# Optimization experiments

Measured on AMD Instinct MI355X. Metric: run time of the kernel, lower is better.

The kernel has to match this reference:

```python
import jax, jax.numpy as jnp
import numpy as np

INPUT_DIM = 512
LATENT_DIM = 64
H1, H2 = 128, 64  # hardcoded hidden widths in Encoder/Decoder
BATCH = 4096


def _xavier(key, shape):
    fan_out, fan_in = shape
    std = jnp.sqrt(2.0 / (fan_in + fan_out))
    return std * jax.random.normal(key, shape, dtype=jnp.float32)


def setup_inputs() -> dict:
    key = jax.random.key(0)
    ks = jax.random.split(key, 10)
    d = LATENT_DIM
    n_pairs = d * (d - 1) // 2
    n_funcs = 1 + d + n_pairs  # bias + states + pairwise products
    inp = {
        "x": jax.random.normal(ks[0], (BATCH, INPUT_DIM), dtype=jnp.float32),
        "xdot": jax.random.normal(ks[1], (BATCH, INPUT_DIM), dtype=jnp.float32),
        # encoder weights (torch Linear layout: [out, in])
        "We1": _xavier(ks[2], (H1, INPUT_DIM)), "be1": jnp.zeros((H1,), jnp.float32),
        "We2": _xavier(ks[3], (H2, H1)),        "be2": jnp.zeros((H2,), jnp.float32),
        "We3": _xavier(ks[4], (d, H2)),         "be3": jnp.zeros((d,), jnp.float32),
        # decoder weights
        "Wd1": _xavier(ks[5], (H2, d)),         "bd1": jnp.zeros((H2,), jnp.float32),
        "Wd2": _xavier(ks[6], (H1, H2)),        "bd2": jnp.zeros((H1,), jnp.float32),
        "Wd3": _xavier(ks[7], (INPUT_DIM, H1)), "bd3": jnp.zeros((INPUT_DIM,), jnp.float32),
        "XI": jnp.ones((n_funcs, d), jnp.float32),
        "XI_mask": jnp.ones((n_funcs, d), jnp.float32),
    }
    return inp


def _mlp_with_jacobian(x, Ws, bs):
    """3-layer relu MLP; returns output and per-sample analytic Jacobian [B,out,in].
    Jacobian = diag(m3) W3 diag(m2) W2 diag(m1) W1 with relu masks m_l."""
    h = x
    J = None
    for W, b in zip(Ws, bs):
        h = h @ W.T + b                      # [B, out_l]
        m = (h > 0).astype(h.dtype)          # relu mask (grad 0 at 0, matching torch)
        h = jnp.maximum(h, 0)
        Wm = m[:, :, None] * W[None]         # [B, out_l, in_l]
        J = Wm if J is None else jnp.einsum('boh,bhi->boi', Wm, J)
    return h, J


def _sindy_library(z):
    B, d = z.shape
    iu, ju = np.triu_indices(d, k=1)
    ones = jnp.ones((B, 1), z.dtype)
    pairs = z[:, iu] * z[:, ju]              # [B, d(d-1)/2]
    return jnp.concatenate([ones, z, pairs], axis=1)


def reference(x, xdot, We1, be1, We2, be2, We3, be3,
              Wd1, bd1, Wd2, bd2, Wd3, bd3, XI, XI_mask):
    z, Jenc = _mlp_with_jacobian(x, (We1, We2, We3), (be1, be2, be3))
    dz_dt = jnp.einsum('bli,bi->bl', Jenc, xdot)
    xh, Jdec = _mlp_with_jacobian(z, (Wd1, Wd2, Wd3), (bd1, bd2, bd3))
    theta = _sindy_library(z)
    dz_dt_sindy = theta @ (XI_mask * XI)
    dxh_dt = jnp.einsum('bol,bl->bo', Jdec, dz_dt_sindy)
    return (xh, dxh_dt, z, dz_dt, dz_dt_sindy)
```

## Files before the change

kernel.cpp:

```cpp
#include <hip/hip_runtime.h>

#define BATCH 4096
#define IN_DIM 512
#define H1DIM 128
#define H2DIM 64
#define DDIM 64
#define NFUNC 2081
#define NFPAD 2112
#define CHUNK 704
#define KS_PER_CHUNK 22

typedef short bf16x8 __attribute__((ext_vector_type(8)));
typedef float f32x4 __attribute__((ext_vector_type(4)));
#define MFMA(a,b,c) __builtin_amdgcn_mfma_f32_16x16x32_bf16(a,b,c,0,0,0)

#define WSZ1 (H1DIM*IN_DIM)
#define WSZ2 (H2DIM*H1DIM)
#define WSZ3 (DDIM*H2DIM)
#define WSZ4 (H2DIM*DDIM)
#define WSZ5 (H1DIM*H2DIM)
#define WSZ6 (IN_DIM*H1DIM)

__device__ __forceinline__ short f2b(float f) {
    union { float f; unsigned u; } x; x.f = f;
    unsigned r = x.u + 0x7fffu + ((x.u >> 16) & 1u);
    return (short)(r >> 16);
}
__device__ __forceinline__ float b2f(short s) {
    union { unsigned u; float f; } x; x.u = ((unsigned)(unsigned short)s) << 16;
    return x.f;
}
__device__ __forceinline__ void split3f(float v, short& s0, short& s1, short& s2) {
    s0 = f2b(v); float r = v - b2f(s0);
    s1 = f2b(r); float r2 = r - b2f(s1);
    s2 = f2b(r2);
}

__device__ __forceinline__ void st_b16(short* t, int RS, int r, int c, short v) {
    int b = (c * 2) ^ ((r & 7) << 4);
    *(short*)((char*)(t + r * RS) + b) = v;
}
__device__ __forceinline__ void st_b32s(short* t, int RS, int r, int c, unsigned v) {
    int b = (c * 2) ^ ((r & 7) << 4);
    *(unsigned*)((char*)(t + r * RS) + b) = v;
}
__device__ __forceinline__ void st_b128(short* t, int RS, int r, int c0, bf16x8 v) {
    int b = (c0 * 2) ^ ((r & 7) << 4);
    *(bf16x8*)((char*)(t + r * RS) + b) = v;
}
__device__ __forceinline__ bf16x8 ld_af(const short* t, int RS, int lane, int kbase) {
    int r = lane & 15;
    int b = ((kbase + (lane >> 4) * 8) * 2) ^ ((r & 7) << 4);
    return *(const bf16x8*)((const char*)(t + r * RS) + b);
}
__device__ __forceinline__ bf16x8 ld_bp(const short* P, int blk, int lane) {
    return *(const bf16x8*)(P + ((size_t)blk * 64 + lane) * 8);
}

__device__ __forceinline__ void mf9(bf16x8 f0, bf16x8 f1, bf16x8 f2, bf16x8 fv,
                                    bf16x8 b0, bf16x8 b1, bf16x8 b2,
                                    f32x4& P, f32x4& Q, f32x4& V) {
    P = MFMA(f0, b0, P); Q = MFMA(f1, b1, Q);
    P = MFMA(f1, b0, P); Q = MFMA(f0, b1, Q);
    P = MFMA(f2, b0, P); Q = MFMA(f2, b1, Q);
    P = MFMA(f0, b2, P); Q = MFMA(f1, b2, Q);
    V = MFMA(fv, b0, V);
}

__device__ __forceinline__ void epi_store(short* t0, short* t1, short* t2, short* tv, int RS,
                                          int lane, int col, const f32x4& P, const f32x4& Q,
                                          const f32x4& V, float bb)
{
    #pragma unroll
    for (int q = 0; q < 4; ++q) {
        int row = (lane >> 4) * 4 + q;
        float pre = P[q] + Q[q] + bb;
        float h = fmaxf(pre, 0.f);
        short s0, s1, s2;
        split3f(h, s0, s1, s2);
        st_b16(t0, RS, row, col, s0);
        st_b16(t1, RS, row, col, s1);
        st_b16(t2, RS, row, col, s2);
        st_b16(tv, RS, row, col, pre > 0.f ? f2b(V[q]) : (short)0);
    }
}

template<int K>
__device__ void pack_w(const float* __restrict__ W, short* __restrict__ dst, int NK,
                       int gid, int nthr)
{
    for (int o = gid; o < NK / 8; o += nthr) {
        int c = o / (K / 8), k0 = (o - c * (K / 8)) * 8;
        int cb = c >> 4, ks = k0 >> 5;
        int L = (((k0 >> 3) & 3) << 4) | (c & 15);
        int idx = ((cb * (K / 32) + ks) * 64 + L) * 8;
        union { short s[8]; bf16x8 v; } p0, p1, p2;
        #pragma unroll
        for (int j = 0; j < 8; ++j)
            split3f(W[(size_t)c * K + k0 + j], p0.s[j], p1.s[j], p2.s[j]);
        *(bf16x8*)(dst + idx) = p0.v;
        *(bf16x8*)(dst + NK + idx) = p1.v;
        *(bf16x8*)(dst + 2 * NK + idx) = p2.v;
    }
}

__global__ void initk(const float* __restrict__ We1, const float* __restrict__ We2,
                      const float* __restrict__ We3, const float* __restrict__ Wd1,
                      const float* __restrict__ Wd2, const float* __restrict__ Wd3,
                      const float* __restrict__ XI, const float* __restrict__ XIm,
                      short* Wp1, short* Wp2, short* Wp3, short* Wp4, short* Wp5, short* Wp6,
                      short* xiP, int2* pk)
{
    int gid = blockIdx.x * blockDim.x + threadIdx.x;
    int nthr = gridDim.x * blockDim.x;

    pack_w<512>(We1, Wp1, WSZ1, gid, nthr);
    pack_w<128>(We2, Wp2, WSZ2, gid, nthr);
    pack_w<64>(We3, Wp3, WSZ3, gid, nthr);
    pack_w<64>(Wd1, Wp4, WSZ4, gid, nthr);
    pack_w<64>(Wd2, Wp5, WSZ5, gid, nthr);
    pack_w<128>(Wd3, Wp6, WSZ6, gid, nthr);

    for (int i = gid; i < 4 * 66 * 64; i += nthr) {
        int cb = i / (66 * 64);
        int r = i - cb * (66 * 64);
        int ks = r >> 6, L = r & 63;
        int col = cb * 16 + (L & 15);
        union { short s[8]; bf16x8 v; } w;
        #pragma unroll
        for (int j = 0; j < 8; ++j) {
            int f = ks * 32 + ((L >> 4) << 3) + j;
            float v = (f < NFUNC) ? XI[(size_t)f * DDIM + col] * XIm[(size_t)f * DDIM + col] : 0.f;
            w.s[j] = f2b(v);
        }
        *(bf16x8*)(xiP + (size_t)i * 8) = w.v;
    }

    for (int f = gid; f < NFPAD; f += nthr) {
        int a, b;
        if (f == 0) { a = 64; b = 64; }
        else if (f <= DDIM) { a = f - 1; b = 64; }
        else if (f < NFUNC) {
            int p = f - 1 - DDIM; int i2 = 0, cum = 0;
            while (cum + (63 - i2) <= p) { cum += 63 - i2; ++i2; }
            a = i2; b = i2 + 1 + (p - cum);
        } else { a = 65; b = 65; }
        pk[f] = make_int2(a, b);
    }
}

__global__ __launch_bounds__(512, 2)
void fused(const float* __restrict__ x, const float* __restrict__ xdot,
           const float* __restrict__ be1, const float* __restrict__ be2,
           const float* __restrict__ be3, const float* __restrict__ bd1,
           const float* __restrict__ bd2, const float* __restrict__ bd3,
           const short* __restrict__ Wp1, const short* __restrict__ Wp2,
           const short* __restrict__ Wp3, const short* __restrict__ Wp4,
           const short* __restrict__ Wp5, const short* __restrict__ Wp6,
           const short* __restrict__ xiP, const int2* __restrict__ pk,
           float* __restrict__ xh, float* __restrict__ dxh, float* __restrict__ zo,
           float* __restrict__ dz, float* __restrict__ dzs)
{
    __shared__ __align__(16) char ldsbuf[57600];
    short* h1s0 = (short*)(ldsbuf + 0);
    short* h1s1 = (short*)(ldsbuf + 4096);
    short* h1s2 = (short*)(ldsbuf + 8192);
    short* v1   = (short*)(ldsbuf + 12288);
    short* xs0  = (short*)(ldsbuf + 16384);
    short* xs1  = (short*)(ldsbuf + 24576);
    short* xs2  = (short*)(ldsbuf + 32768);
    short* xsv  = (short*)(ldsbuf + 40960);
    short* h2s0 = (short*)(ldsbuf + 16384);
    short* h2s1 = (short*)(ldsbuf + 18432);
    short* h2s2 = (short*)(ldsbuf + 20480);
    short* v2   = (short*)(ldsbuf + 22528);
    short* th0  = (short*)(ldsbuf + 0);
    short* th1  = (short*)(ldsbuf + 22528);
    float* rbuf = (float*)(ldsbuf + 16384);
    short* g1s0 = (short*)(ldsbuf + 0);
    short* g1s1 = (short*)(ldsbuf + 2048);
    short* g1s2 = (short*)(ldsbuf + 4096);
    short* u1   = (short*)(ldsbuf + 6144);
    short* g2s0 = (short*)(ldsbuf + 8192);
    short* g2s1 = (short*)(ldsbuf + 12288);
    short* g2s2 = (short*)(ldsbuf + 16384);
    short* u2   = (short*)(ldsbuf + 20480);
    short* zb0  = (short*)(ldsbuf + 45056);
    short* zb1  = (short*)(ldsbuf + 47104);
    short* zb2  = (short*)(ldsbuf + 49152);
    short* dzsb = (short*)(ldsbuf + 51200);
    float* zf   = (float*)(ldsbuf + 53248);

    const int tid = threadIdx.x, lane = tid & 63, wave = tid >> 6;
    const int wq = wave & 3;
    const int row0 = blockIdx.x * 16;
    const int c16 = lane & 15;
    const int tr = tid & 15, bg = tid >> 4;
    const int tf = bg * 22;
    const int scb = wave & 3, skh = wave >> 2;

    float bb1 = be1[wave * 16 + c16];
    float bb2 = be2[wq * 16 + c16];
    float bb3 = be3[wq * 16 + c16];
    float bD1 = bd1[wq * 16 + c16];
    float bD2 = bd2[wave * 16 + c16];
    float bD3[4];
    #pragma unroll
    for (int i = 0; i < 4; ++i) bD3[i] = bd3[wave * 64 + i * 16 + c16];

    f32x4 P1 = {}, Q1 = {}, V1 = {};
    {
        const int srow = tid >> 5, sc0 = (tid & 31) * 8;
        const float* xr  = x    + (size_t)(row0 + srow) * IN_DIM + sc0;
        const float* xdr = xdot + (size_t)(row0 + srow) * IN_DIM + sc0;
        #pragma clang loop unroll(disable)
        for (int h = 0; h < 2; ++h) {
            {
                f32x4 va = *(const f32x4*)(xr + h * 256);
                f32x4 vb = *(const f32x4*)(xr + h * 256 + 4);
                f32x4 da = *(const f32x4*)(xdr + h * 256);
                f32x4 db = *(const f32x4*)(xdr + h * 256 + 4);
                union { short s[8]; bf16x8 v; } a0, a1, a2, dv;
                #pragma unroll
                for (int j = 0; j < 4; ++j) {
                    split3f(va[j], a0.s[j], a1.s[j], a2.s[j]);
                    split3f(vb[j], a0.s[j + 4], a1.s[j + 4], a2.s[j + 4]);
                    dv.s[j] = f2b(da[j]); dv.s[j + 4] = f2b(db[j]);
                }
                st_b128(xs0, 256, srow, sc0, a0.v);
                st_b128(xs1, 256, srow, sc0, a1.v);
                st_b128(xs2, 256, srow, sc0, a2.v);
                st_b128(xsv, 256, srow, sc0, dv.v);
            }
            __syncthreads();
            bf16x8 B0[2], B1[2], B2[2];
#define LB(ks, sl) { int blk = wave * 16 + h * 8 + (ks); \
            B0[sl] = ld_bp(Wp1, blk, lane); B1[sl] = ld_bp(Wp1 + WSZ1, blk, lane); \
            B2[sl] = ld_bp(Wp1 + 2 * WSZ1, blk, lane); }
            LB(0, 0)
            #pragma unroll
            for (int ks = 0; ks < 8; ++ks) {
                if (ks < 7) LB(ks + 1, (ks + 1) & 1)
                bf16x8 f0 = ld_af(xs0, 256, lane, ks * 32);
                bf16x8 f1 = ld_af(xs1, 256, lane, ks * 32);
                bf16x8 f2 = ld_af(xs2, 256, lane, ks * 32);
                bf16x8 fv = ld_af(xsv, 256, lane, ks * 32);
                mf9(f0, f1, f2, fv, B0[ks & 1], B1[ks & 1], B2[ks & 1], P1, Q1, V1);
            }
#undef LB
            __syncthreads();
        }
        epi_store(h1s0, h1s1, h1s2, v1, 128, lane, wave * 16 + c16, P1, Q1, V1, bb1);
    }
    bf16x8 L2B[4][3];
    if (wave < 4) {
        #pragma unroll
        for (int ks = 0; ks < 4; ++ks) {
            int blk = wq * 4 + ks;
            L2B[ks][0] = ld_bp(Wp2, blk, lane);
            L2B[ks][1] = ld_bp(Wp2 + WSZ2, blk, lane);
            L2B[ks][2] = ld_bp(Wp2 + 2 * WSZ2, blk, lane);
        }
    }
    __syncthreads();

    bf16x8 L3B[2][3];
    if (wave < 4) {
        bf16x8 Aa[4][4];
        #pragma unroll
        for (int ks = 0; ks < 4; ++ks) {
            Aa[ks][0] = ld_af(h1s0, 128, lane, ks * 32);
            Aa[ks][1] = ld_af(h1s1, 128, lane, ks * 32);
            Aa[ks][2] = ld_af(h1s2, 128, lane, ks * 32);
            Aa[ks][3] = ld_af(v1, 128, lane, ks * 32);
        }
        #pragma unroll
        for (int ks = 0; ks < 2; ++ks) {
            int blk = wq * 2 + ks;
            L3B[ks][0] = ld_bp(Wp3, blk, lane);
            L3B[ks][1] = ld_bp(Wp3 + WSZ3, blk, lane);
            L3B[ks][2] = ld_bp(Wp3 + 2 * WSZ3, blk, lane);
        }
        f32x4 P = {}, Q = {}, V = {};
        #pragma unroll
        for (int ks = 0; ks < 4; ++ks)
            mf9(Aa[ks][0], Aa[ks][1], Aa[ks][2], Aa[ks][3], L2B[ks][0], L2B[ks][1], L2B[ks][2], P, Q, V);
        epi_store(h2s0, h2s1, h2s2, v2, 64, lane, wq * 16 + c16, P, Q, V, bb2);
    }
    __syncthreads();

    bf16x8 X[11];
    if (wave < 4) {
        bf16x8 Aa[2][4];
        #pragma unroll
        for (int ks = 0; ks < 2; ++ks) {
            Aa[ks][0] = ld_af(h2s0, 64, lane, ks * 32);
            Aa[ks][1] = ld_af(h2s1, 64, lane, ks * 32);
            Aa[ks][2] = ld_af(h2s2, 64, lane, ks * 32);
            Aa[ks][3] = ld_af(v2, 64, lane, ks * 32);
        }
        f32x4 P = {}, Q = {}, V = {};
        #pragma unroll
        for (int ks = 0; ks < 2; ++ks)
            mf9(Aa[ks][0], Aa[ks][1], Aa[ks][2], Aa[ks][3], L3B[ks][0], L3B[ks][1], L3B[ks][2], P, Q, V);
        int col = wq * 16 + c16;
        #pragma unroll
        for (int q = 0; q < 4; ++q) {
            int row = (lane >> 4) * 4 + q;
            float pre = P[q] + Q[q] + bb3;
            float hz = fmaxf(pre, 0.f);
            float vz = pre > 0.f ? V[q] : 0.f;
            zf[row * 68 + col] = hz;
            short s0, s1, s2;
            split3f(hz, s0, s1, s2);
            st_b16(zb0, 64, row, col, s0);
            st_b16(zb1, 64, row, col, s1);
            st_b16(zb2, 64, row, col, s2);
            zo[(size_t)(row0 + row) * DDIM + col] = hz;
            dz[(size_t)(row0 + row) * DDIM + col] = vz;
        }
        if (tid < 32) { int r = tid & 15; zf[r * 68 + 64 + (tid >> 4)] = (tid >> 4) ? 0.f : 1.f; }
    }
    #pragma unroll
    for (int kk = 0; kk < 11; ++kk)
        X[kk] = ld_bp(xiP, scb * 66 + skh * 11 + kk, lane);
    __syncthreads();

    f32x4 sa = {};
    auto build = [&](int ch, short* t) {
        #pragma clang loop unroll(disable)
        for (int j = 0; j < 11; ++j) {
            int f0 = ch * CHUNK + tf + 2 * j;
            int2 p0 = pk[f0], p1 = pk[f0 + 1];
            float t0 = zf[tr * 68 + p0.x] * zf[tr * 68 + p0.y];
            float t1 = zf[tr * 68 + p1.x] * zf[tr * 68 + p1.y];
            unsigned u = (unsigned)(unsigned short)f2b(t0)
                       | ((unsigned)(unsigned short)f2b(t1) << 16);
            st_b32s(t, 704, tr, tf + 2 * j, u);
        }
    };
#define SMF(t) { _Pragma("unroll") for (int kk = 0; kk < 11; ++kk) { \
        bf16x8 a = ld_af(t, 704, lane, (skh * 11 + kk) * 32); \
        sa = MFMA(a, X[kk], sa); } }
#define ISX(ch) { _Pragma("unroll") for (int kk = 0; kk < 11; ++kk) \
        X[kk] = ld_bp(xiP, scb * 66 + (ch) * KS_PER_CHUNK + skh * 11 + kk, lane); }

    build(0, th0);
    __syncthreads();
    SMF(th0) ISX(1) build(1, th1);
    __syncthreads();
    SMF(th1) ISX(2) build(2, th0);
    __syncthreads();
    SMF(th0)
    if (wave >= 4) *(f32x4*)&rbuf[(scb * 64 + lane) * 4] = sa;
    __syncthreads();
    bf16x8 D1B[2][3];
    if (wave < 4) {
        f32x4 sacc = sa + *(const f32x4*)&rbuf[(scb * 64 + lane) * 4];
        #pragma unroll
        for (int ks = 0; ks < 2; ++ks) {
            int blk = wq * 2 + ks;
            D1B[ks][0] = ld_bp(Wp4, blk, lane);
            D1B[ks][1] = ld_bp(Wp4 + WSZ4, blk, lane);
            D1B[ks][2] = ld_bp(Wp4 + 2 * WSZ4, blk, lane);
        }
        int col = wq * 16 + c16;
        #pragma unroll
        for (int q = 0; q < 4; ++q) {
            int row = (lane >> 4) * 4 + q;
            float v = sacc[q];
            dzs[(size_t)(row0 + row) * DDIM + col] = v;
            st_b16(dzsb, 64, row, col, f2b(v));
        }
    }
#undef SMF
#undef ISX
    __syncthreads();

    bf16x8 D2B[2][3];
    if (wave < 4) {
        bf16x8 Aa[2][4];
        #pragma unroll
        for (int ks = 0; ks < 2; ++ks) {
            Aa[ks][0] = ld_af(zb0, 64, lane, ks * 32);
            Aa[ks][1] = ld_af(zb1, 64, lane, ks * 32);
            Aa[ks][2] = ld_af(zb2, 64, lane, ks * 32);
            Aa[ks][3] = ld_af(dzsb, 64, lane, ks * 32);
        }
        f32x4 P = {}, Q = {}, V = {};
        #pragma unroll
        for (int ks = 0; ks < 2; ++ks)
            mf9(Aa[ks][0], Aa[ks][1], Aa[ks][2], Aa[ks][3], D1B[ks][0], D1B[ks][1], D1B[ks][2], P, Q, V);
        epi_store(g1s0, g1s1, g1s2, u1, 64, lane, wq * 16 + c16, P, Q, V, bD1);
    }
    #pragma unroll
    for (int ks = 0; ks < 2; ++ks) {
        int blk = wave * 2 + ks;
        D2B[ks][0] = ld_bp(Wp5, blk, lane);
        D2B[ks][1] = ld_bp(Wp5 + WSZ5, blk, lane);
        D2B[ks][2] = ld_bp(Wp5 + 2 * WSZ5, blk, lane);
    }
    __syncthreads();

    {
        bf16x8 Aa[2][4];
        #pragma unroll
        for (int ks = 0; ks < 2; ++ks) {
            Aa[ks][0] = ld_af(g1s0, 64, lane, ks * 32);
            Aa[ks][1] = ld_af(g1s1, 64, lane, ks * 32);
            Aa[ks][2] = ld_af(g1s2, 64, lane, ks * 32);
            Aa[ks][3] = ld_af(u1, 64, lane, ks * 32);
        }
        f32x4 P = {}, Q = {}, V = {};
        #pragma unroll
        for (int ks = 0; ks < 2; ++ks)
            mf9(Aa[ks][0], Aa[ks][1], Aa[ks][2], Aa[ks][3], D2B[ks][0], D2B[ks][1], D2B[ks][2], P, Q, V);
        epi_store(g2s0, g2s1, g2s2, u2, 128, lane, wave * 16 + c16, P, Q, V, bD2);
    }
    __syncthreads();

    {
        f32x4 P[4] = {}, Q[4] = {}, V[4] = {};
        bf16x8 Bp[4][3];
        bf16x8 Ax0[2], Ax1[2], Ax2[2], Axv[2];
#define D3_LA(ks, b) { Ax0[b] = ld_af(g2s0, 128, lane, (ks) * 32); Ax1[b] = ld_af(g2s1, 128, lane, (ks) * 32); \
                       Ax2[b] = ld_af(g2s2, 128, lane, (ks) * 32); Axv[b] = ld_af(u2, 128, lane, (ks) * 32); }
#define D3_LB(s, sl) { int blk = (wave * 4 + ((s) & 3)) * 4 + ((s) >> 2); \
        Bp[sl][0] = ld_bp(Wp6, blk, lane); Bp[sl][1] = ld_bp(Wp6 + WSZ6, blk, lane); \
        Bp[sl][2] = ld_bp(Wp6 + 2 * WSZ6, blk, lane); }
        D3_LA(0, 0)
        D3_LB(0, 0) D3_LB(1, 1) D3_LB(2, 2) D3_LB(3, 3)
        #pragma unroll
        for (int ks = 0; ks < 4; ++ks) {
            if (ks < 3) D3_LA(ks + 1, (ks + 1) & 1)
            #pragma unroll
            for (int cf = 0; cf < 4; ++cf) {
                const int s = ks * 4 + cf, sl = s & 3;
                mf9(Ax0[ks & 1], Ax1[ks & 1], Ax2[ks & 1], Axv[ks & 1],
                    Bp[sl][0], Bp[sl][1], Bp[sl][2], P[cf], Q[cf], V[cf]);
                if (s + 4 < 16) D3_LB(s + 4, sl)
            }
        }
#undef D3_LA
#undef D3_LB
        #pragma unroll
        for (int cf = 0; cf < 4; ++cf) {
            int col = wave * 64 + cf * 16 + c16;
            float bb = bD3[cf];
            #pragma unroll
            for (int q = 0; q < 4; ++q) {
                int row = (lane >> 4) * 4 + q;
                float pre = P[cf][q] + Q[cf][q] + bb;
                xh[(size_t)(row0 + row) * IN_DIM + col] = fmaxf(pre, 0.f);
                dxh[(size_t)(row0 + row) * IN_DIM + col] = pre > 0.f ? V[cf][q] : 0.f;
            }
        }
    }
}

extern "C" void kernel_launch(void* const* d_in, const int* in_sizes, int n_in,
                              void* d_out, int out_size, void* d_ws, size_t ws_size,
                              hipStream_t stream)
{
    const float* x    = (const float*)d_in[0];
    const float* xdot = (const float*)d_in[1];
    const float* We1  = (const float*)d_in[2];
    const float* be1  = (const float*)d_in[3];
    const float* We2  = (const float*)d_in[4];
    const float* be2  = (const float*)d_in[5];
    const float* We3  = (const float*)d_in[6];
    const float* be3  = (const float*)d_in[7];
    const float* Wd1  = (const float*)d_in[8];
    const float* bd1  = (const float*)d_in[9];
    const float* Wd2  = (const float*)d_in[10];
    const float* bd2  = (const float*)d_in[11];
    const float* Wd3  = (const float*)d_in[12];
    const float* bd3  = (const float*)d_in[13];
    const float* XI   = (const float*)d_in[14];
    const float* XIm  = (const float*)d_in[15];

    float* out = (float*)d_out;
    float* xh  = out;
    float* dxh = out + (size_t)BATCH * IN_DIM;
    float* zo  = dxh + (size_t)BATCH * IN_DIM;
    float* dz  = zo + (size_t)BATCH * DDIM;
    float* dzs = dz + (size_t)BATCH * DDIM;

    int2*  pk  = (int2*)d_ws;
    short* Wp1 = (short*)(pk + NFPAD);
    short* Wp2 = Wp1 + 3 * WSZ1;
    short* Wp3 = Wp2 + 3 * WSZ2;
    short* Wp4 = Wp3 + 3 * WSZ3;
    short* Wp5 = Wp4 + 3 * WSZ4;
    short* Wp6 = Wp5 + 3 * WSZ5;
    short* xiP = Wp6 + 3 * WSZ6;

    initk<<<256, 256, 0, stream>>>(We1, We2, We3, Wd1, Wd2, Wd3, XI, XIm,
                                   Wp1, Wp2, Wp3, Wp4, Wp5, Wp6, xiP, pk);
    fused<<<BATCH / 16, 512, 0, stream>>>(x, xdot, be1, be2, be3, bd1, bd2, bd3,
                                          Wp1, Wp2, Wp3, Wp4, Wp5, Wp6, xiP, pk,
                                          xh, dxh, zo, dz, dzs);
}
```

Measured before the change: 42.90 us.

## Prefetch both input halves upfront and split layer-2 K across all eight waves

All global loads of x and xdot for both K-halves of layer 1 are now issued at the start instead of inside the loop, so the second half's memory latency overlaps with the first half's MFMA work. Layer 2 previously ran on only four waves. It now splits the K dimension across all eight waves, and partial accumulators from the upper waves are reduced through an LDS scratch buffer. This costs more live registers, an extra LDS round-trip and an extra barrier.

Result: no change. 42.66 us (-0.6%).

```diff
diff --git a/kernel.cpp b/kernel.cpp
--- a/kernel.cpp
+++ b/kernel.cpp
@@ -177,6 +177,7 @@
     short* th0  = (short*)(ldsbuf + 0);
     short* th1  = (short*)(ldsbuf + 22528);
     float* rbuf = (float*)(ldsbuf + 16384);
+    float* l2rb = (float*)(ldsbuf + 32768);
     short* g1s0 = (short*)(ldsbuf + 0);
     short* g1s1 = (short*)(ldsbuf + 2048);
     short* g1s2 = (short*)(ldsbuf + 4096);
@@ -213,79 +214,98 @@
         const int srow = tid >> 5, sc0 = (tid & 31) * 8;
         const float* xr  = x    + (size_t)(row0 + srow) * IN_DIM + sc0;
         const float* xdr = xdot + (size_t)(row0 + srow) * IN_DIM + sc0;
-        #pragma clang loop unroll(disable)
-        for (int h = 0; h < 2; ++h) {
-            {
-                f32x4 va = *(const f32x4*)(xr + h * 256);
-                f32x4 vb = *(const f32x4*)(xr + h * 256 + 4);
-                f32x4 da = *(const f32x4*)(xdr + h * 256);
-                f32x4 db = *(const f32x4*)(xdr + h * 256 + 4);
-                union { short s[8]; bf16x8 v; } a0, a1, a2, dv;
-                #pragma unroll
-                for (int j = 0; j < 4; ++j) {
-                    split3f(va[j], a0.s[j], a1.s[j], a2.s[j]);
-                    split3f(vb[j], a0.s[j + 4], a1.s[j + 4], a2.s[j + 4]);
-                    dv.s[j] = f2b(da[j]); dv.s[j + 4] = f2b(db[j]);
-                }
-                st_b128(xs0, 256, srow, sc0, a0.v);
-                st_b128(xs1, 256, srow, sc0, a1.v);
-                st_b128(xs2, 256, srow, sc0, a2.v);
-                st_b128(xsv, 256, srow, sc0, dv.v);
+        f32x4 va0 = *(const f32x4*)(xr);        f32x4 vb0 = *(const f32x4*)(xr + 4);
+        f32x4 da0 = *(const f32x4*)(xdr);       f32x4 db0 = *(const f32x4*)(xdr + 4);
+        f32x4 va1 = *(const f32x4*)(xr + 256);  f32x4 vb1 = *(const f32x4*)(xr + 260);
+        f32x4 da1 = *(const f32x4*)(xdr + 256); f32x4 db1 = *(const f32x4*)(xdr + 260);
+
+#define L1_STAGE(va, vb, da, db) { \
+        union { short s[8]; bf16x8 v; } a0, a1, a2, dv; \
+        _Pragma("unroll") \
+        for (int j = 0; j < 4; ++j) { \
+            split3f((va)[j], a0.s[j], a1.s[j], a2.s[j]); \
+            split3f((vb)[j], a0.s[j + 4], a1.s[j + 4], a2.s[j + 4]); \
+            dv.s[j] = f2b((da)[j]); dv.s[j + 4] = f2b((db)[j]); \
+        } \
+        st_b128(xs0, 256, srow, sc0, a0.v); \
+        st_b128(xs1, 256, srow, sc0, a1.v); \
+        st_b128(xs2, 256, srow, sc0, a2.v); \
+        st_b128(xsv, 256, srow, sc0, dv.v); }
+
+#define L1_COMP(h) { \
+        bf16x8 B0[2], B1[2], B2[2]; \
+        { int blk = wave * 16 + (h) * 8; \
+          B0[0] = ld_bp(Wp1, blk, lane); B1[0] = ld_bp(Wp1 + WSZ1, blk, lane); \
+          B2[0] = ld_bp(Wp1 + 2 * WSZ1, blk, lane); } \
+        _Pragma("unroll") \
+        for (int ks = 0; ks < 8; ++ks) { \
+            if (ks < 7) { int blk = wave * 16 + (h) * 8 + ks + 1; \
+                B0[(ks + 1) & 1] = ld_bp(Wp1, blk, lane); \
+                B1[(ks + 1) & 1] = ld_bp(Wp1 + WSZ1, blk, lane); \
+                B2[(ks + 1) & 1] = ld_bp(Wp1 + 2 * WSZ1, blk, lane); } \
+            bf16x8 f0 = ld_af(xs0, 256, lane, ks * 32); \
+            bf16x8 f1 = ld_af(xs1, 256, lane, ks * 32); \
+            bf16x8 f2 = ld_af(xs2, 256, lane, ks * 32); \
+            bf16x8 fv = ld_af(xsv, 256, lane, ks * 32); \
+            mf9(f0, f1, f2, fv, B0[ks & 1], B1[ks & 1], B2[ks & 1], P1, Q1, V1); \
+        } }
+
+        L1_STAGE(va0, vb0, da0, db0)
+        __syncthreads();
+        L1_COMP(0)
+        __syncthreads();
+        L1_STAGE(va1, vb1, da1, db1)
+        __syncthreads();
+        L1_COMP(1)
+        __syncthreads();
+#undef L1_STAGE
+#undef L1_COMP
+        epi_store(h1s0, h1s1, h1s2, v1, 128, lane, wave * 16 + c16, P1, Q1, V1, bb1);
+    }
+    bf16x8 L2B[2][3];
+    #pragma unroll
+    for (int ks = 0; ks < 2; ++ks) {
+        int blk = wq * 4 + (wave >> 2) * 2 + ks;
+        L2B[ks][0] = ld_bp(Wp2, blk, lane);
+        L2B[ks][1] = ld_bp(Wp2 + WSZ2, blk, lane);
+        L2B[ks][2] = ld_bp(Wp2 + 2 * WSZ2, blk, lane);
+    }
+    __syncthreads();
+
+    bf16x8 L3B[2][3];
+    {
+        const int kh = wave >> 2;
+        f32x4 P = {}, Q = {}, V = {};
+        #pragma unroll
+        for (int ks = 0; ks < 2; ++ks) {
+            int kg = kh * 2 + ks;
+            bf16x8 a0 = ld_af(h1s0, 128, lane, kg * 32);
+            bf16x8 a1 = ld_af(h1s1, 128, lane, kg * 32);
+            bf16x8 a2 = ld_af(h1s2, 128, lane, kg * 32);
+            bf16x8 av = ld_af(v1, 128, lane, kg * 32);
+            mf9(a0, a1, a2, av, L2B[ks][0], L2B[ks][1], L2B[ks][2], P, Q, V);
+        }
+        if (kh == 1) {
+            float* rb = l2rb + (wq * 64 + lane) * 12;
+            *(f32x4*)(rb) = P; *(f32x4*)(rb + 4) = Q; *(f32x4*)(rb + 8) = V;
+        }
+        if (wave < 4) {
+            #pragma unroll
+            for (int ks = 0; ks < 2; ++ks) {
+                int blk = wq * 2 + ks;
+                L3B[ks][0] = ld_bp(Wp3, blk, lane);
+                L3B[ks][1] = ld_bp(Wp3 + WSZ3, blk, lane);
+                L3B[ks][2] = ld_bp(Wp3 + 2 * WSZ3, blk, lane);
             }
-            __syncthreads();
-            bf16x8 B0[2], B1[2], B2[2];
-#define LB(ks, sl) { int blk = wave * 16 + h * 8 + (ks); \
-            B0[sl] = ld_bp(Wp1, blk, lane); B1[sl] = ld_bp(Wp1 + WSZ1, blk, lane); \
-            B2[sl] = ld_bp(Wp1 + 2 * WSZ1, blk, lane); }
-            LB(0, 0)
-            #pragma unroll
-            for (int ks = 0; ks < 8; ++ks) {
-                if (ks < 7) LB(ks + 1, (ks + 1) & 1)
-                bf16x8 f0 = ld_af(xs0, 256, lane, ks * 32);
-                bf16x8 f1 = ld_af(xs1, 256, lane, ks * 32);
-                bf16x8 f2 = ld_af(xs2, 256, lane, ks * 32);
-                bf16x8 fv = ld_af(xsv, 256, lane, ks * 32);
-                mf9(f0, f1, f2, fv, B0[ks & 1], B1[ks & 1], B2[ks & 1], P1, Q1, V1);
-            }
-#undef LB
-            __syncthreads();
-        }
-        epi_store(h1s0, h1s1, h1s2, v1, 128, lane, wave * 16 + c16, P1, Q1, V1, bb1);
-    }
-    bf16x8 L2B[4][3];
-    if (wave < 4) {
-        #pragma unroll
-        for (int ks = 0; ks < 4; ++ks) {
-            int blk = wq * 4 + ks;
-            L2B[ks][0] = ld_bp(Wp2, blk, lane);
-            L2B[ks][1] = ld_bp(Wp2 + WSZ2, blk, lane);
-            L2B[ks][2] = ld_bp(Wp2 + 2 * WSZ2, blk, lane);
-        }
-    }
-    __syncthreads();
-
-    bf16x8 L3B[2][3];
-    if (wave < 4) {
-        bf16x8 Aa[4][4];
-        #pragma unroll
-        for (int ks = 0; ks < 4; ++ks) {
-            Aa[ks][0] = ld_af(h1s0, 128, lane, ks * 32);
-            Aa[ks][1] = ld_af(h1s1, 128, lane, ks * 32);
-            Aa[ks][2] = ld_af(h1s2, 128, lane, ks * 32);
-            Aa[ks][3] = ld_af(v1, 128, lane, ks * 32);
-        }
-        #pragma unroll
-        for (int ks = 0; ks < 2; ++ks) {
-            int blk = wq * 2 + ks;
-            L3B[ks][0] = ld_bp(Wp3, blk, lane);
-            L3B[ks][1] = ld_bp(Wp3 + WSZ3, blk, lane);
-            L3B[ks][2] = ld_bp(Wp3 + 2 * WSZ3, blk, lane);
-        }
-        f32x4 P = {}, Q = {}, V = {};
-        #pragma unroll
-        for (int ks = 0; ks < 4; ++ks)
-            mf9(Aa[ks][0], Aa[ks][1], Aa[ks][2], Aa[ks][3], L2B[ks][0], L2B[ks][1], L2B[ks][2], P, Q, V);
-        epi_store(h2s0, h2s1, h2s2, v2, 64, lane, wq * 16 + c16, P, Q, V, bb2);
+        }
+        __syncthreads();
+        if (wave < 4) {
+            const float* rb = l2rb + (wq * 64 + lane) * 12;
+            f32x4 P2 = P + *(const f32x4*)(rb);
+            f32x4 Q2 = Q + *(const f32x4*)(rb + 4);
+            f32x4 V2 = V + *(const f32x4*)(rb + 8);
+            epi_store(h2s0, h2s1, h2s2, v2, 64, lane, wq * 16 + c16, P2, Q2, V2, bb2);
+        }
     }
     __syncthreads();
 
```

## Stage full 512-wide input tile in LDS at once, removing K-half loop

Applied to the files above, without the earlier changes.

The first layer used to stage x/xdot in two 256-column halves, with a barrier pair per half. It now issues all global loads for both halves up front and converts them to bf16 splits into a full 512-wide LDS tile. It then runs a single 16-step MFMA loop. LDS is enlarged to 64 KB and all buffers are remapped to fit, removing one round of barriers and exposing more memory-level parallelism at the cost of more registers and LDS, which may reduce occupancy below two blocks per CU.

After: 42.46 us (median of 2 runs). Within noise of the previous version (-1.0%).

```diff
diff --git a/kernel.cpp b/kernel.cpp
--- a/kernel.cpp
+++ b/kernel.cpp
@@ -161,22 +161,27 @@
            float* __restrict__ xh, float* __restrict__ dxh, float* __restrict__ zo,
            float* __restrict__ dz, float* __restrict__ dzs)
 {
-    __shared__ __align__(16) char ldsbuf[57600];
+    __shared__ __align__(16) char ldsbuf[65536];
+    short* xs0  = (short*)(ldsbuf + 0);
+    short* xs1  = (short*)(ldsbuf + 16384);
+    short* xs2  = (short*)(ldsbuf + 32768);
+    short* xsv  = (short*)(ldsbuf + 49152);
     short* h1s0 = (short*)(ldsbuf + 0);
     short* h1s1 = (short*)(ldsbuf + 4096);
     short* h1s2 = (short*)(ldsbuf + 8192);
     short* v1   = (short*)(ldsbuf + 12288);
-    short* xs0  = (short*)(ldsbuf + 16384);
-    short* xs1  = (short*)(ldsbuf + 24576);
-    short* xs2  = (short*)(ldsbuf + 32768);
-    short* xsv  = (short*)(ldsbuf + 40960);
     short* h2s0 = (short*)(ldsbuf + 16384);
     short* h2s1 = (short*)(ldsbuf + 18432);
     short* h2s2 = (short*)(ldsbuf + 20480);
     short* v2   = (short*)(ldsbuf + 22528);
-    short* th0  = (short*)(ldsbuf + 0);
-    short* th1  = (short*)(ldsbuf + 22528);
-    float* rbuf = (float*)(ldsbuf + 16384);
+    short* zb0  = (short*)(ldsbuf + 24576);
+    short* zb1  = (short*)(ldsbuf + 26624);
+    short* zb2  = (short*)(ldsbuf + 28672);
+    short* dzsb = (short*)(ldsbuf + 30720);
+    float* zf   = (float*)(ldsbuf + 32768);
+    short* th0  = (short*)(ldsbuf + 37888);
+    short* th1  = (short*)(ldsbuf + 0);
+    float* rbuf = (float*)(ldsbuf + 60416);
     short* g1s0 = (short*)(ldsbuf + 0);
     short* g1s1 = (short*)(ldsbuf + 2048);
     short* g1s2 = (short*)(ldsbuf + 4096);
@@ -185,11 +190,6 @@
     short* g2s1 = (short*)(ldsbuf + 12288);
     short* g2s2 = (short*)(ldsbuf + 16384);
     short* u2   = (short*)(ldsbuf + 20480);
-    short* zb0  = (short*)(ldsbuf + 45056);
-    short* zb1  = (short*)(ldsbuf + 47104);
-    short* zb2  = (short*)(ldsbuf + 49152);
-    short* dzsb = (short*)(ldsbuf + 51200);
-    float* zf   = (float*)(ldsbuf + 53248);
 
     const int tid = threadIdx.x, lane = tid & 63, wave = tid >> 6;
     const int wq = wave & 3;
@@ -213,43 +213,58 @@
         const int srow = tid >> 5, sc0 = (tid & 31) * 8;
         const float* xr  = x    + (size_t)(row0 + srow) * IN_DIM + sc0;
         const float* xdr = xdot + (size_t)(row0 + srow) * IN_DIM + sc0;
-        #pragma clang loop unroll(disable)
-        for (int h = 0; h < 2; ++h) {
-            {
-                f32x4 va = *(const f32x4*)(xr + h * 256);
-                f32x4 vb = *(const f32x4*)(xr + h * 256 + 4);
-                f32x4 da = *(const f32x4*)(xdr + h * 256);
-                f32x4 db = *(const f32x4*)(xdr + h * 256 + 4);
-                union { short s[8]; bf16x8 v; } a0, a1, a2, dv;
-                #pragma unroll
-                for (int j = 0; j < 4; ++j) {
-                    split3f(va[j], a0.s[j], a1.s[j], a2.s[j]);
-                    split3f(vb[j], a0.s[j + 4], a1.s[j + 4], a2.s[j + 4]);
-                    dv.s[j] = f2b(da[j]); dv.s[j + 4] = f2b(db[j]);
-                }
-                st_b128(xs0, 256, srow, sc0, a0.v);
-                st_b128(xs1, 256, srow, sc0, a1.v);
-                st_b128(xs2, 256, srow, sc0, a2.v);
-                st_b128(xsv, 256, srow, sc0, dv.v);
+        f32x4 va0 = *(const f32x4*)(xr);        f32x4 vb0 = *(const f32x4*)(xr + 4);
+        f32x4 da0 = *(const f32x4*)(xdr);       f32x4 db0 = *(const f32x4*)(xdr + 4);
+        f32x4 va1 = *(const f32x4*)(xr + 256);  f32x4 vb1 = *(const f32x4*)(xr + 260);
+        f32x4 da1 = *(const f32x4*)(xdr + 256); f32x4 db1 = *(const f32x4*)(xdr + 260);
+        {
+            union { short s[8]; bf16x8 v; } a0, a1, a2, dv;
+            #pragma unroll
+            for (int j = 0; j < 4; ++j) {
+                split3f(va0[j], a0.s[j], a1.s[j], a2.s[j]);
+                split3f(vb0[j], a0.s[j + 4], a1.s[j + 4], a2.s[j + 4]);
+                dv.s[j] = f2b(da0[j]); dv.s[j + 4] = f2b(db0[j]);
             }
-            __syncthreads();
-            bf16x8 B0[2], B1[2], B2[2];
-#define LB(ks, sl) { int blk = wave * 16 + h * 8 + (ks); \
-            B0[sl] = ld_bp(Wp1, blk, lane); B1[sl] = ld_bp(Wp1 + WSZ1, blk, lane); \
-            B2[sl] = ld_bp(Wp1 + 2 * WSZ1, blk, lane); }
-            LB(0, 0)
+            st_b128(xs0, 512, srow, sc0, a0.v);
+            st_b128(xs1, 512, srow, sc0, a1.v);
+            st_b128(xs2, 512, srow, sc0, a2.v);
+            st_b128(xsv, 512, srow, sc0, dv.v);
+        }
+        {
+            union { short s[8]; bf16x8 v; } a0, a1, a2, dv;
             #pragma unroll
-            for (int ks = 0; ks < 8; ++ks) {
-                if (ks < 7) LB(ks + 1, (ks + 1) & 1)
-                bf16x8 f0 = ld_af(xs0, 256, lane, ks * 32);
-                bf16x8 f1 = ld_af(xs1, 256, lane, ks * 32);
-                bf16x8 f2 = ld_af(xs2, 256, lane, ks * 32);
-                bf16x8 fv = ld_af(xsv, 256, lane, ks * 32);
-                mf9(f0, f1, f2, fv, B0[ks & 1], B1[ks & 1], B2[ks & 1], P1, Q1, V1);
+            for (int j = 0; j < 4; ++j) {
+                split3f(va1[j], a0.s[j], a1.s[j], a2.s[j]);
+                split3f(vb1[j], a0.s[j + 4], a1.s[j + 4], a2.s[j + 4]);
+                dv.s[j] = f2b(da1[j]); dv.s[j + 4] = f2b(db1[j]);
             }
-#undef LB
-            __syncthreads();
-        }
+            st_b128(xs0, 512, srow, sc0 + 256, a0.v);
+            st_b128(xs1, 512, srow, sc0 + 256, a1.v);
+            st_b128(xs2, 512, srow, sc0 + 256, a2.v);
+            st_b128(xsv, 512, srow, sc0 + 256, dv.v);
+        }
+        __syncthreads();
+        bf16x8 B0[2], B1[2], B2[2];
+        {
+            int blk = wave * 16;
+            B0[0] = ld_bp(Wp1, blk, lane); B1[0] = ld_bp(Wp1 + WSZ1, blk, lane);
+            B2[0] = ld_bp(Wp1 + 2 * WSZ1, blk, lane);
+        }
+        #pragma unroll
+        for (int ks = 0; ks < 16; ++ks) {
+            if (ks < 15) {
+                int blk = wave * 16 + ks + 1;
+                B0[(ks + 1) & 1] = ld_bp(Wp1, blk, lane);
+                B1[(ks + 1) & 1] = ld_bp(Wp1 + WSZ1, blk, lane);
+                B2[(ks + 1) & 1] = ld_bp(Wp1 + 2 * WSZ1, blk, lane);
+            }
+            bf16x8 f0 = ld_af(xs0, 512, lane, ks * 32);
+            bf16x8 f1 = ld_af(xs1, 512, lane, ks * 32);
+            bf16x8 f2 = ld_af(xs2, 512, lane, ks * 32);
+            bf16x8 fv = ld_af(xsv, 512, lane, ks * 32);
+            mf9(f0, f1, f2, fv, B0[ks & 1], B1[ks & 1], B2[ks & 1], P1, Q1, V1);
+        }
+        __syncthreads();
         epi_store(h1s0, h1s1, h1s2, v1, 128, lane, wave * 16 + c16, P1, Q1, V1, bb1);
     }
     bf16x8 L2B[4][3];
```
